# Kernel optimization log

Measured on AMD Instinct MI355X. Metric: run time of the kernel, lower is better.

The kernel has to match this reference:

```python
import jax, jax.numpy as jnp
import numpy as np

SP = 4      # sp_size (number of simulated sequence-parallel ranks)
NH = 16     # num_attention_heads
HD = 64     # head_dim
HS = 1024   # hidden_size
B = 1       # batch
S = 8192    # global sequence length (SP chunks of 2048)


def setup_inputs() -> dict:
    key = jax.random.key(0)
    ks = jax.random.split(key, 9)
    w_scale = 1.0 / np.sqrt(HS)
    def w(k):
        # xavier-ish init, stored as [in, out] so y = x @ W + b
        return jax.random.uniform(k, (HS, HS), jnp.float32, -w_scale, w_scale)
    return {
        'hidden_states': jax.random.normal(ks[0], (B, S, HS), jnp.float32),
        'Wq': w(ks[1]), 'bq': jnp.zeros((HS,), jnp.float32),
        'Wk': w(ks[2]), 'bk': jnp.zeros((HS,), jnp.float32),
        'Wv': w(ks[3]), 'bv': jnp.zeros((HS,), jnp.float32),
        'Wo': w(ks[4]), 'bo': jnp.zeros((HS,), jnp.float32),
    }


def reference(hidden_states, Wq, bq, Wk, bk, Wv, bv, Wo, bo):
    b, s, _ = hidden_states.shape
    sc = s // SP  # per-rank chunk length
    inv_sqrt_hd = 1.0 / np.sqrt(HD)

    def heads(x):
        # [B, S, HS] -> [SP, B, NH, Sc, HD]
        return x.reshape(b, SP, sc, NH, HD).transpose(1, 0, 3, 2, 4)

    q = heads(hidden_states @ Wq + bq)
    k = heads(hidden_states @ Wk + bk)
    v = heads(hidden_states @ Wv + bv)

    out = jnp.zeros_like(q)
    # ring attention: at step i each rank r attends to chunk (r + i) mod SP
    for i in range(SP):
        ki = jnp.roll(k, -i, axis=0)
        vi = jnp.roll(v, -i, axis=0)
        scores = jnp.einsum('sbhqd,sbhkd->sbhqk', q, ki) * inv_sqrt_hd
        probs = jax.nn.softmax(scores, axis=-1)  # per-chunk softmax (faithful to source)
        out = out + jnp.einsum('sbhqk,sbhkd->sbhqd', probs, vi)
    out = out / SP  # source divides accumulated context by sp_size

    # [SP, B, NH, Sc, HD] -> [B, S, NH*HD]
    ctx = out.transpose(1, 0, 3, 2, 4).reshape(b, s, NH * HD)
    return ctx @ Wo + bo
```

## Files before the change

### kernel.cpp

```cpp
#include <hip/hip_runtime.h>

#define DEVINL __device__ __forceinline__

typedef __attribute__((ext_vector_type(8))) short short8;
typedef __attribute__((ext_vector_type(4))) float floatx4;
typedef __attribute__((ext_vector_type(2))) unsigned uintx2;

DEVINL unsigned short f2bf(float f){
  unsigned u = __builtin_bit_cast(unsigned, f);
  u += 0x7FFFu + ((u >> 16) & 1u);
  return (unsigned short)(u >> 16);
}
DEVINL unsigned pk2(float a, float b){
  unsigned ua = __builtin_bit_cast(unsigned, a);
  unsigned ub = __builtin_bit_cast(unsigned, b);
  ua += 0x7FFFu + ((ua >> 16) & 1u);
  ub += 0x7FFFu + ((ub >> 16) & 1u);
  return (ua >> 16) | (ub & 0xFFFF0000u);
}
DEVINL unsigned pkfast(float a, float b){
  unsigned ua = __builtin_bit_cast(unsigned, a) + 0x8000u;
  unsigned ub = __builtin_bit_cast(unsigned, b) + 0x8000u;
  return __builtin_amdgcn_perm(ub, ua, 0x07060302u);
}
DEVINL float bf2f(unsigned short h){
  unsigned u = ((unsigned)h) << 16;
  return __builtin_bit_cast(float, u);
}
DEVINL void gload_lds16(const void* g, void* l){
  __builtin_amdgcn_global_load_lds((const __attribute__((address_space(1))) void*)g,
                                   (__attribute__((address_space(3))) void*)l, 16, 0, 0);
}
DEVINL int perm2(int k){
  return (((k >> 4) & 1) << 5) | (((k >> 2) & 3) << 3) | (((k >> 5) & 1) << 2) | (k & 3);
}

__global__ void k_detect(const unsigned* __restrict__ w, int* __restrict__ flag){
  __shared__ int cnt;
  if (threadIdx.x == 0) cnt = 0;
  __syncthreads();
  int c = 0;
  for (int i = threadIdx.x; i < 1024; i += 256){
    unsigned e = (w[i] >> 7) & 0xFFu;
    c += (e >= 120u && e <= 132u) ? 1 : 0;
  }
  atomicAdd(&cnt, c);
  __syncthreads();
  if (threadIdx.x == 0) *flag = (cnt > 512) ? 1 : 0;
}

__global__ void k_conv_bf16(const void* __restrict__ src, unsigned short* __restrict__ dst,
                            int n, const int* __restrict__ flag){
  int i = (blockIdx.x * 256 + threadIdx.x) * 8;
  if (i >= n) return;
  if (*flag){
    ((uint4*)dst)[i >> 3] = ((const uint4*)src)[i >> 3];
  } else {
    const float* s = (const float*)src;
    short8 v;
    #pragma unroll
    for (int j = 0; j < 8; j++) v[j] = (short)f2bf(s[i + j]);
    *(short8*)(dst + i) = v;
  }
}

__global__ void k_conv_wT4(const void* __restrict__ s0, const void* __restrict__ s1,
                           const void* __restrict__ s2, const void* __restrict__ s3,
                           unsigned short* __restrict__ d0, unsigned short* __restrict__ d1,
                           unsigned short* __restrict__ d2, unsigned short* __restrict__ d3,
                           const int* __restrict__ flag){
  __shared__ float tile[32][33];
  const void* src; unsigned short* dst;
  switch (blockIdx.z){
    case 0: src = s0; dst = d0; break;
    case 1: src = s1; dst = d1; break;
    case 2: src = s2; dst = d2; break;
    default: src = s3; dst = d3; break;
  }
  const int tx = threadIdx.x & 31, ty = threadIdx.x >> 5;
  const int bx = blockIdx.x, by = blockIdx.y;
  const int isbf = *flag;
  #pragma unroll
  for (int r = 0; r < 32; r += 8){
    int k = by*32 + ty + r, n = bx*32 + tx;
    float v = isbf ? bf2f(((const unsigned short*)src)[k*1024 + n])
                   : ((const float*)src)[k*1024 + n];
    tile[ty + r][tx] = v;
  }
  __syncthreads();
  #pragma unroll
  for (int r = 0; r < 32; r += 8){
    int n = bx*32 + ty + r, k = by*32 + tx;
    dst[n*1024 + k] = f2bf(tile[tx][ty + r]);
  }
}

__global__ void k_conv_b4(const void* __restrict__ s0, const void* __restrict__ s1,
                          const void* __restrict__ s2, const void* __restrict__ s3,
                          float* __restrict__ dst, const int* __restrict__ flag){
  int i = blockIdx.x * 256 + threadIdx.x;
  if (i >= 4096) return;
  int z = i >> 10, j = i & 1023;
  const void* s = (z == 0) ? s0 : (z == 1) ? s1 : (z == 2) ? s2 : s3;
  dst[i] = (*flag) ? bf2f(((const unsigned short*)s)[j]) : ((const float*)s)[j];
}

template<int MODE>
__global__ __launch_bounds__(256, 2) void k_gemm(
    const unsigned short* __restrict__ A, const unsigned short* __restrict__ Bt,
    const float* __restrict__ bias, void* __restrict__ C0, void* __restrict__ C1,
    void* __restrict__ C2, const int* __restrict__ flagp, float scale)
{
  const int K = 1024;
  __shared__ __align__(16) unsigned short As[128*32];
  __shared__ __align__(16) unsigned short Bs[128*32];
  const int tid = threadIdx.x;
  const int lane = tid & 63, wave = tid >> 6;
  const int quad = lane >> 4, l15 = lane & 15;
  const int m0 = blockIdx.x * 128, n0 = blockIdx.y * 128;
  const int wm = (wave >> 1) * 64, wn = (wave & 1) * 64;
  const floatx4 fzero = {0.f, 0.f, 0.f, 0.f};
  floatx4 acc[4][4];
  #pragma unroll
  for (int i = 0; i < 4; i++)
    #pragma unroll
    for (int j = 0; j < 4; j++) acc[i][j] = fzero;

  for (int k0 = 0; k0 < K; k0 += 32){
    __syncthreads();
    #pragma unroll
    for (int rep = 0; rep < 2; rep++){
      int idx = tid + rep*256;
      int row = idx >> 2, c = idx & 3;
      gload_lds16(A  + (size_t)(m0 + row)*K + (k0 + c*8), &As[idx*8]);
      gload_lds16(Bt + (size_t)(n0 + row)*K + (k0 + c*8), &Bs[idx*8]);
    }
    asm volatile("s_waitcnt vmcnt(0)" ::: "memory");
    __syncthreads();
    short8 af[4], bf[4];
    #pragma unroll
    for (int i = 0; i < 4; i++) af[i] = *(const short8*)&As[(wm + i*16 + l15)*32 + quad*8];
    #pragma unroll
    for (int j = 0; j < 4; j++) bf[j] = *(const short8*)&Bs[(wn + j*16 + l15)*32 + quad*8];
    #pragma unroll
    for (int i = 0; i < 4; i++)
      #pragma unroll
      for (int j = 0; j < 4; j++)
        acc[i][j] = __builtin_amdgcn_mfma_f32_16x16x32_bf16(af[i], bf[j], acc[i][j], 0, 0, 0);
  }

  float bs[4];
  #pragma unroll
  for (int j = 0; j < 4; j++) bs[j] = bias[n0 + wn + j*16 + l15];
  const int useBf = (MODE == 1) ? *flagp : 1;
  #pragma unroll
  for (int i = 0; i < 4; i++){
    #pragma unroll
    for (int j = 0; j < 4; j++){
      int n = n0 + wn + j*16 + l15;
      #pragma unroll
      for (int r = 0; r < 4; r++){
        int m = m0 + wm + i*16 + quad*4 + r;
        float v = acc[i][j][r] + bs[j];
        if (MODE == 3){
          int sel = n >> 10, nn = n & 1023;
          if (sel == 0){
            int dd = (nn & 63) ^ ((m & 7) << 3);
            ((unsigned short*)C0)[((size_t)(nn >> 6)*8192 + m)*64 + dd] = f2bf(v * scale);
          } else if (sel == 1){
            int dd = (nn & 63) ^ ((m & 7) << 3);
            ((unsigned short*)C1)[((size_t)(nn >> 6)*8192 + m)*64 + dd] = f2bf(v);
          } else {
            int s2 = perm2(m & 63) ^ ((nn & 7) << 3);
            ((unsigned short*)C2)[(size_t)nn*8192 + (m & ~63) + s2] = f2bf(v);
          }
        } else {
          if (useBf) ((unsigned short*)C0)[(size_t)m*1024 + n] = f2bf(v);
          else       ((float*)C0)[(size_t)m*1024 + n] = v;
        }
      }
    }
  }
}

__global__ __launch_bounds__(256, 2) void k_attn(
    const unsigned short* __restrict__ Qg, const unsigned short* __restrict__ Kg,
    const unsigned short* __restrict__ Vg, unsigned short* __restrict__ ctx)
{
  __shared__ __align__(16) unsigned short Qs[256*64];
  __shared__ __align__(16) unsigned short Ks[2][64*64];
  __shared__ __align__(16) unsigned short Vs[2][64*64];
  const int tid = threadIdx.x, lane = tid & 63, wave = tid >> 6;
  const int quad = lane >> 4, l15 = lane & 15;
  const int bid = blockIdx.x;
  const int xcd = bid & 7, slot = bid >> 3;
  const int h = xcd*2 + (slot >> 5);
  const int rem = slot & 31, rchunk = rem >> 3, qt = rem & 7;
  const int sq0 = rchunk*2048 + qt*256;
  const char* Qbase = (const char*)(Qg + (size_t)h*8192*64 + (size_t)sq0*64);
  const char* Kbase = (const char*)(Kg + (size_t)h*8192*64);
  const char* Vbase = (const char*)(Vg + (size_t)h*8192*64);
  const int wq0 = wave * 64;
  const floatx4 fzero = {0.f, 0.f, 0.f, 0.f};

  const int idx0 = tid, idx1 = tid + 256;
  const size_t voff0 = (size_t)(idx0 >> 3)*16384 + (idx0 & 7)*16;
  const size_t voff1 = (size_t)(idx1 >> 3)*16384 + (idx1 & 7)*16;

  auto stage = [&](int buf, int kvs){
    const char* Kt = Kbase + (size_t)kvs*128;
    const char* Vt = Vbase + (size_t)kvs*2;
    char* kd = (char*)Ks[buf];
    char* vd = (char*)Vs[buf];
    gload_lds16(Kt + idx0*16, kd + idx0*16);
    gload_lds16(Kt + idx1*16, kd + idx1*16);
    gload_lds16(Vt + voff0, vd + idx0*16);
    gload_lds16(Vt + voff1, vd + idx1*16);
  };

  #pragma unroll
  for (int rep = 0; rep < 8; rep++){
    int idx = tid + rep*256;
    gload_lds16(Qbase + idx*16, (char*)Qs + idx*16);
  }
  stage(0, rchunk*2048);
  asm volatile("s_waitcnt vmcnt(0)" ::: "memory");
  __syncthreads();

  short8 qf[4][2];
  #pragma unroll
  for (int mi = 0; mi < 4; mi++)
    #pragma unroll
    for (int ks = 0; ks < 2; ks++){
      int row = wq0 + mi*16 + l15;
      qf[mi][ks] = *(const short8*)&Qs[row*64 + (((ks*4 + quad) ^ (row & 7)))*8];
    }

  short8 ones;
  #pragma unroll
  for (int j = 0; j < 8; j++) ones[j] = (short)0x3F80;

  floatx4 Of[4][4];
  #pragma unroll
  for (int mi = 0; mi < 4; mi++)
    #pragma unroll
    for (int di = 0; di < 4; di++) Of[mi][di] = fzero;

  for (int i = 0; i < 4; i++){
    floatx4 Oc[4][4], Ol[4];
    #pragma unroll
    for (int mi = 0; mi < 4; mi++){
      Ol[mi] = fzero;
      #pragma unroll
      for (int di = 0; di < 4; di++) Oc[mi][di] = fzero;
    }

    for (int kt = 0; kt < 32; kt++){
      const int t = i*32 + kt, cur = t & 1;
      asm volatile("s_waitcnt vmcnt(0)" ::: "memory");
      __syncthreads();
      if (t < 127){
        int t1 = t + 1;
        int kvs = ((rchunk + (t1 >> 5)) & 3)*2048 + (t1 & 31)*64;
        stage(cur ^ 1, kvs);
      }

      short8 pf[4][2];
      #pragma unroll
      for (int mi = 0; mi < 4; mi++){
        floatx4 St[4];
        #pragma unroll
        for (int ni = 0; ni < 4; ni++) St[ni] = fzero;
        #pragma unroll
        for (int ks = 0; ks < 2; ks++)
          #pragma unroll
          for (int ni = 0; ni < 4; ni++){
            int krow = ni*16 + l15;
            short8 kf = *(const short8*)&Ks[cur][krow*64 + (((ks*4 + quad) ^ (krow & 7)))*8];
            St[ni] = __builtin_amdgcn_mfma_f32_16x16x32_bf16(kf, qf[mi][ks], St[ni], 0, 0, 0);
          }
        #pragma unroll
        for (int ni = 0; ni < 4; ni++)
          #pragma unroll
          for (int r = 0; r < 4; r++)
            St[ni][r] = __builtin_amdgcn_exp2f(St[ni][r]);
        #pragma unroll
        for (int ks = 0; ks < 2; ks++){
          uintx2 lo, hi;
          lo[0] = pkfast(St[ks  ][0], St[ks  ][1]);
          lo[1] = pkfast(St[ks  ][2], St[ks  ][3]);
          hi[0] = pkfast(St[2+ks][0], St[2+ks][1]);
          hi[1] = pkfast(St[2+ks][2], St[2+ks][3]);
          union { uintx2 u[2]; short8 s; } cv;
          cv.u[0] = lo; cv.u[1] = hi;
          pf[mi][ks] = cv.s;
        }
      }

      #pragma unroll
      for (int ks = 0; ks < 2; ks++){
        #pragma unroll
        for (int di = 0; di < 4; di++){
          int vrow = di*16 + l15;
          short8 vf = *(const short8*)&Vs[cur][vrow*64 + (((ks*4 + quad) ^ (vrow & 7)))*8];
          #pragma unroll
          for (int mi = 0; mi < 4; mi++)
            Oc[mi][di] = __builtin_amdgcn_mfma_f32_16x16x32_bf16(vf, pf[mi][ks], Oc[mi][di], 0, 0, 0);
        }
        #pragma unroll
        for (int mi = 0; mi < 4; mi++)
          Ol[mi] = __builtin_amdgcn_mfma_f32_16x16x32_bf16(ones, pf[mi][ks], Ol[mi], 0, 0, 0);
      }
    }

    #pragma unroll
    for (int mi = 0; mi < 4; mi++){
      float inv = __builtin_amdgcn_rcpf(Ol[mi][0]);
      #pragma unroll
      for (int di = 0; di < 4; di++)
        #pragma unroll
        for (int r = 0; r < 4; r++) Of[mi][di][r] += Oc[mi][di][r] * inv;
    }
  }

  #pragma unroll
  for (int mi = 0; mi < 4; mi++){
    int q = sq0 + wq0 + mi*16 + l15;
    #pragma unroll
    for (int di = 0; di < 4; di++){
      uintx2 w;
      w[0] = pk2(Of[mi][di][0]*0.25f, Of[mi][di][1]*0.25f);
      w[1] = pk2(Of[mi][di][2]*0.25f, Of[mi][di][3]*0.25f);
      *(uintx2*)&ctx[(size_t)q*1024 + h*64 + di*16 + quad*4] = w;
    }
  }
}

extern "C" void kernel_launch(void* const* d_in, const int* in_sizes, int n_in,
                              void* d_out, int out_size, void* d_ws, size_t ws_size,
                              hipStream_t stream)
{
  (void)in_sizes; (void)n_in; (void)out_size; (void)ws_size;
  char* ws = (char*)d_ws;
  size_t off = 0;
  auto alloc = [&](size_t bytes) -> char* {
    char* p = ws + off;
    off = (off + bytes + 255) & ~(size_t)255;
    return p;
  };
  int* flag            = (int*)alloc(4);
  unsigned short* hsb  = (unsigned short*)alloc((size_t)8192*1024*2);
  unsigned short* wqt  = (unsigned short*)alloc((size_t)1024*1024*2);
  unsigned short* wkt  = (unsigned short*)alloc((size_t)1024*1024*2);
  unsigned short* wvt  = (unsigned short*)alloc((size_t)1024*1024*2);
  unsigned short* wot  = (unsigned short*)alloc((size_t)1024*1024*2);
  float* biasAll       = (float*)alloc(4096*4);
  unsigned short* Qb   = (unsigned short*)alloc((size_t)16*8192*64*2);
  unsigned short* Kb   = (unsigned short*)alloc((size_t)16*8192*64*2);
  unsigned short* Vb   = (unsigned short*)alloc((size_t)16*8192*64*2);
  unsigned short* ctxb = (unsigned short*)alloc((size_t)8192*1024*2);

  k_detect<<<1, 256, 0, stream>>>((const unsigned*)d_in[0], flag);
  k_conv_bf16<<<4096, 256, 0, stream>>>(d_in[0], hsb, 8192*1024, flag);
  k_conv_wT4<<<dim3(32,32,4), 256, 0, stream>>>(d_in[1], d_in[3], d_in[5], d_in[7],
                                                wqt, wkt, wvt, wot, flag);
  k_conv_b4<<<16, 256, 0, stream>>>(d_in[2], d_in[4], d_in[6], d_in[8], biasAll, flag);

  const float Cs = 0.18033688011112042f;
  k_gemm<3><<<dim3(64, 24), 256, 0, stream>>>(hsb, wqt, biasAll, Qb, Kb, Vb, nullptr, Cs);

  k_attn<<<512, 256, 0, stream>>>(Qb, Kb, Vb, ctxb);

  k_gemm<1><<<dim3(64, 8), 256, 0, stream>>>(ctxb, wot, biasAll + 3072, d_out,
                                             nullptr, nullptr, flag, 1.0f);
}
```

Measured before the change: 472.9 us.

## Split attention work over eight waves per block with fewer query rows each

```diff
diff --git a/kernel.cpp b/kernel.cpp
--- a/kernel.cpp
+++ b/kernel.cpp
@@ -22,6 +22,19 @@
   unsigned ua = __builtin_bit_cast(unsigned, a) + 0x8000u;
   unsigned ub = __builtin_bit_cast(unsigned, b) + 0x8000u;
   return __builtin_amdgcn_perm(ub, ua, 0x07060302u);
+}
+DEVINL unsigned pkbf(float a, float b){
+#if defined(__has_builtin)
+#if __has_builtin(__builtin_amdgcn_cvt_pk_bf16_f32)
+  typedef __attribute__((ext_vector_type(2))) __bf16 bf16x2_t;
+  bf16x2_t r = __builtin_amdgcn_cvt_pk_bf16_f32(a, b);
+  return __builtin_bit_cast(unsigned, r);
+#else
+  return pkfast(a, b);
+#endif
+#else
+  return pkfast(a, b);
+#endif
 }
 DEVINL float bf2f(unsigned short h){
   unsigned u = ((unsigned)h) << 16;
@@ -183,7 +196,7 @@
   }
 }
 
-__global__ __launch_bounds__(256, 2) void k_attn(
+__global__ __launch_bounds__(512, 4) void k_attn(
     const unsigned short* __restrict__ Qg, const unsigned short* __restrict__ Kg,
     const unsigned short* __restrict__ Vg, unsigned short* __restrict__ ctx)
 {
@@ -200,36 +213,28 @@
   const char* Qbase = (const char*)(Qg + (size_t)h*8192*64 + (size_t)sq0*64);
   const char* Kbase = (const char*)(Kg + (size_t)h*8192*64);
   const char* Vbase = (const char*)(Vg + (size_t)h*8192*64);
-  const int wq0 = wave * 64;
-  const floatx4 fzero = {0.f, 0.f, 0.f, 0.f};
-
-  const int idx0 = tid, idx1 = tid + 256;
-  const size_t voff0 = (size_t)(idx0 >> 3)*16384 + (idx0 & 7)*16;
-  const size_t voff1 = (size_t)(idx1 >> 3)*16384 + (idx1 & 7)*16;
+  const int wq0 = wave * 32;
+  const floatx4 fz = {0.f, 0.f, 0.f, 0.f};
+
+  const size_t voff = (size_t)(tid >> 3)*16384 + (size_t)(tid & 7)*16;
 
   auto stage = [&](int buf, int kvs){
-    const char* Kt = Kbase + (size_t)kvs*128;
-    const char* Vt = Vbase + (size_t)kvs*2;
-    char* kd = (char*)Ks[buf];
-    char* vd = (char*)Vs[buf];
-    gload_lds16(Kt + idx0*16, kd + idx0*16);
-    gload_lds16(Kt + idx1*16, kd + idx1*16);
-    gload_lds16(Vt + voff0, vd + idx0*16);
-    gload_lds16(Vt + voff1, vd + idx1*16);
+    gload_lds16(Kbase + (size_t)kvs*128 + tid*16, (char*)Ks[buf] + tid*16);
+    gload_lds16(Vbase + (size_t)kvs*2 + voff,     (char*)Vs[buf] + tid*16);
   };
 
   #pragma unroll
-  for (int rep = 0; rep < 8; rep++){
-    int idx = tid + rep*256;
+  for (int rep = 0; rep < 4; rep++){
+    int idx = tid + rep*512;
     gload_lds16(Qbase + idx*16, (char*)Qs + idx*16);
   }
   stage(0, rchunk*2048);
   asm volatile("s_waitcnt vmcnt(0)" ::: "memory");
   __syncthreads();
 
-  short8 qf[4][2];
-  #pragma unroll
-  for (int mi = 0; mi < 4; mi++)
+  short8 qf[2][2];
+  #pragma unroll
+  for (int mi = 0; mi < 2; mi++)
     #pragma unroll
     for (int ks = 0; ks < 2; ks++){
       int row = wq0 + mi*16 + l15;
@@ -240,19 +245,19 @@
   #pragma unroll
   for (int j = 0; j < 8; j++) ones[j] = (short)0x3F80;
 
-  floatx4 Of[4][4];
-  #pragma unroll
-  for (int mi = 0; mi < 4; mi++)
-    #pragma unroll
-    for (int di = 0; di < 4; di++) Of[mi][di] = fzero;
+  floatx4 Of[2][4];
+  #pragma unroll
+  for (int mi = 0; mi < 2; mi++)
+    #pragma unroll
+    for (int di = 0; di < 4; di++) Of[mi][di] = fz;
 
   for (int i = 0; i < 4; i++){
-    floatx4 Oc[4][4], Ol[4];
-    #pragma unroll
-    for (int mi = 0; mi < 4; mi++){
-      Ol[mi] = fzero;
-      #pragma unroll
-      for (int di = 0; di < 4; di++) Oc[mi][di] = fzero;
+    floatx4 Oc[2][4], Ol[2];
+    #pragma unroll
+    for (int mi = 0; mi < 2; mi++){
+      Ol[mi] = fz;
+      #pragma unroll
+      for (int di = 0; di < 4; di++) Oc[mi][di] = fz;
     }
 
     for (int kt = 0; kt < 32; kt++){
@@ -265,20 +270,22 @@
         stage(cur ^ 1, kvs);
       }
 
-      short8 pf[4][2];
-      #pragma unroll
-      for (int mi = 0; mi < 4; mi++){
+      short8 pf[2][2];
+      #pragma unroll
+      for (int mi = 0; mi < 2; mi++){
         floatx4 St[4];
         #pragma unroll
-        for (int ni = 0; ni < 4; ni++) St[ni] = fzero;
-        #pragma unroll
-        for (int ks = 0; ks < 2; ks++)
-          #pragma unroll
-          for (int ni = 0; ni < 4; ni++){
-            int krow = ni*16 + l15;
-            short8 kf = *(const short8*)&Ks[cur][krow*64 + (((ks*4 + quad) ^ (krow & 7)))*8];
-            St[ni] = __builtin_amdgcn_mfma_f32_16x16x32_bf16(kf, qf[mi][ks], St[ni], 0, 0, 0);
-          }
+        for (int ni = 0; ni < 4; ni++){
+          int krow = ni*16 + l15;
+          short8 kf = *(const short8*)&Ks[cur][krow*64 + ((quad ^ (krow & 7)))*8];
+          St[ni] = __builtin_amdgcn_mfma_f32_16x16x32_bf16(kf, qf[mi][0], fz, 0, 0, 0);
+        }
+        #pragma unroll
+        for (int ni = 0; ni < 4; ni++){
+          int krow = ni*16 + l15;
+          short8 kf = *(const short8*)&Ks[cur][krow*64 + (((4 + quad) ^ (krow & 7)))*8];
+          St[ni] = __builtin_amdgcn_mfma_f32_16x16x32_bf16(kf, qf[mi][1], St[ni], 0, 0, 0);
+        }
         #pragma unroll
         for (int ni = 0; ni < 4; ni++)
           #pragma unroll
@@ -287,10 +294,10 @@
         #pragma unroll
         for (int ks = 0; ks < 2; ks++){
           uintx2 lo, hi;
-          lo[0] = pkfast(St[ks  ][0], St[ks  ][1]);
-          lo[1] = pkfast(St[ks  ][2], St[ks  ][3]);
-          hi[0] = pkfast(St[2+ks][0], St[2+ks][1]);
-          hi[1] = pkfast(St[2+ks][2], St[2+ks][3]);
+          lo[0] = pkbf(St[ks  ][0], St[ks  ][1]);
+          lo[1] = pkbf(St[ks  ][2], St[ks  ][3]);
+          hi[0] = pkbf(St[2+ks][0], St[2+ks][1]);
+          hi[1] = pkbf(St[2+ks][2], St[2+ks][3]);
           union { uintx2 u[2]; short8 s; } cv;
           cv.u[0] = lo; cv.u[1] = hi;
           pf[mi][ks] = cv.s;
@@ -304,17 +311,17 @@
           int vrow = di*16 + l15;
           short8 vf = *(const short8*)&Vs[cur][vrow*64 + (((ks*4 + quad) ^ (vrow & 7)))*8];
           #pragma unroll
-          for (int mi = 0; mi < 4; mi++)
+          for (int mi = 0; mi < 2; mi++)
             Oc[mi][di] = __builtin_amdgcn_mfma_f32_16x16x32_bf16(vf, pf[mi][ks], Oc[mi][di], 0, 0, 0);
         }
         #pragma unroll
-        for (int mi = 0; mi < 4; mi++)
+        for (int mi = 0; mi < 2; mi++)
           Ol[mi] = __builtin_amdgcn_mfma_f32_16x16x32_bf16(ones, pf[mi][ks], Ol[mi], 0, 0, 0);
       }
     }
 
     #pragma unroll
-    for (int mi = 0; mi < 4; mi++){
+    for (int mi = 0; mi < 2; mi++){
       float inv = __builtin_amdgcn_rcpf(Ol[mi][0]);
       #pragma unroll
       for (int di = 0; di < 4; di++)
@@ -324,7 +331,7 @@
   }
 
   #pragma unroll
-  for (int mi = 0; mi < 4; mi++){
+  for (int mi = 0; mi < 2; mi++){
     int q = sq0 + wq0 + mi*16 + l15;
     #pragma unroll
     for (int di = 0; di < 4; di++){
@@ -369,7 +376,7 @@
   const float Cs = 0.18033688011112042f;
   k_gemm<3><<<dim3(64, 24), 256, 0, stream>>>(hsb, wqt, biasAll, Qb, Kb, Vb, nullptr, Cs);
 
-  k_attn<<<512, 256, 0, stream>>>(Qb, Kb, Vb, ctxb);
+  k_attn<<<512, 512, 0, stream>>>(Qb, Kb, Vb, ctxb);
 
   k_gemm<1><<<dim3(64, 8), 256, 0, stream>>>(ctxb, wot, biasAll + 3072, d_out,
                                              nullptr, nullptr, flag, 1.0f);
```

Result: slower. 513.5 us (+8.6%).
